# Kernel tuning notes

Measured on AMD Instinct MI355X. Metric: run time of the kernel, lower is better.

## Reference

```python
import jax, jax.numpy as jnp
import numpy as np

D_MODEL = 1024
NUM_HEADS = 16
D_K = D_MODEL // NUM_HEADS


def setup_inputs() -> dict:
    key = jax.random.key(0)
    ks = jax.random.split(key, 6)
    B, S = 2, 2048
    scale = 1.0 / np.sqrt(D_MODEL)
    x = jax.random.normal(ks[0], (B, S, D_MODEL), dtype=jnp.float32)
    w_q = jax.random.normal(ks[1], (D_MODEL, D_MODEL), dtype=jnp.float32) * scale
    w_k = jax.random.normal(ks[2], (D_MODEL, D_MODEL), dtype=jnp.float32) * scale
    w_v = jax.random.normal(ks[3], (D_MODEL, D_MODEL), dtype=jnp.float32) * scale
    w_o = jax.random.normal(ks[4], (D_MODEL, D_MODEL), dtype=jnp.float32) * scale
    b_o = jax.random.normal(ks[5], (D_MODEL,), dtype=jnp.float32) * 0.01
    return {"x": x, "w_q": w_q, "w_k": w_k, "w_v": w_v, "w_o": w_o, "b_o": b_o}


def reference(x, w_q, w_k, w_v, w_o, b_o):
    B, S, _ = x.shape
    # Linear(d, d, bias=False): y = x @ W.T ; weights stored torch-style [out, in]
    def proj(w):
        y = jnp.einsum('bsd,ed->bse', x, w)
        return y.reshape(B, S, NUM_HEADS, D_K).transpose(0, 2, 1, 3)  # [B,H,S,Dk]
    Q, K, V = proj(w_q), proj(w_k), proj(w_v)
    scores = jnp.einsum('bhqd,bhkd->bhqk', Q, K) / np.sqrt(D_K)
    attn = jax.nn.softmax(scores, axis=-1)  # dropout p=0 (eval) -> identity
    out = jnp.einsum('bhqk,bhkd->bhqd', attn, V)
    out = out.transpose(0, 2, 1, 3).reshape(B, S, D_MODEL)
    return jnp.einsum('bsd,ed->bse', out, w_o) + b_o
```

## Files before the change

### kernel.cpp

```cpp
#include <hip/hip_runtime.h>
#include <hip/hip_bf16.h>


typedef __bf16 bf16x8 __attribute__((ext_vector_type(8)));
typedef float f32x4 __attribute__((ext_vector_type(4)));
typedef float f32x16 __attribute__((ext_vector_type(16)));

__device__ __forceinline__ unsigned short f2bf(float f) {
  union { float f; unsigned int u; } c; c.f = f;
  unsigned int u = c.u;
  return (unsigned short)((u + 0x7FFFu + ((u >> 16) & 1u)) >> 16);
}

__device__ __forceinline__ unsigned int pk2bf(float a, float b) {
  union { float f; unsigned int u; } x, y;
  x.f = a; y.f = b;
  return __builtin_amdgcn_perm(y.u + 0x8000u, x.u + 0x8000u, 0x07060302u);
}

__device__ __forceinline__ bf16x8 ld_frag(const unsigned short* p) {
  union { uint4 u; bf16x8 b; } c;
  c.u = *(const uint4*)p;
  return c.b;
}

__device__ __forceinline__ uint4 cvt8(const float* __restrict__ p) {
  float4 a = *(const float4*)p;
  float4 b = *(const float4*)(p + 4);
  union { uint4 u; unsigned short s[8]; } r;
  r.s[0] = f2bf(a.x); r.s[1] = f2bf(a.y); r.s[2] = f2bf(a.z); r.s[3] = f2bf(a.w);
  r.s[4] = f2bf(b.x); r.s[5] = f2bf(b.y); r.s[6] = f2bf(b.z); r.s[7] = f2bf(b.w);
  return r.u;
}

typedef __attribute__((address_space(1))) const unsigned int as1_u32;
typedef __attribute__((address_space(3))) unsigned int as3_u32;
__device__ __forceinline__ void async16(const unsigned short* g,
                                        unsigned short* l) {
  __builtin_amdgcn_global_load_lds(
      (as1_u32*)(unsigned long long)g,
      (as3_u32*)(unsigned int)(unsigned long long)l, 16, 0, 0);
}

__global__ __launch_bounds__(256) void cvt_all(
    const float* __restrict__ s0, const float* __restrict__ s1,
    const float* __restrict__ s2, const float* __restrict__ s3,
    const float* __restrict__ s4,
    unsigned short* __restrict__ d0, unsigned short* __restrict__ d1,
    unsigned short* __restrict__ d2, unsigned short* __restrict__ d3,
    unsigned short* __restrict__ d4) {
  const float* srcs[5] = {s0, s1, s2, s3, s4};
  unsigned short* dsts[5] = {d0, d1, d2, d3, d4};
  const int ns[5] = {4194304, 1048576, 1048576, 1048576, 1048576};
  const int y = blockIdx.y;
  const int idx = (blockIdx.x * 256 + threadIdx.x) * 8;
  if (idx >= ns[y]) return;
  *(uint4*)(dsts[y] + idx) = cvt8(srcs[y] + idx);
}

template <int BM, bool OUT_F32>
__global__ __launch_bounds__(256, 3) void gemm_bt(
    const unsigned short* __restrict__ A,
    const unsigned short* __restrict__ w0,
    const unsigned short* __restrict__ w1,
    const unsigned short* __restrict__ w2,
    const float* __restrict__ bias,
    void* __restrict__ outraw, float z0scale) {
  constexpr int NT = (BM == 128) ? 4 : 2;
  constexpr int RA = BM / 4;
  const int z = blockIdx.z;
  const unsigned short* W = (z == 0) ? w0 : ((z == 1) ? w1 : w2);
  const float scl = (z == 0) ? z0scale : 1.0f;

  __shared__ unsigned short a_lds[BM * 64];
  __shared__ unsigned short b_lds[128 * 64];

  const int tid = threadIdx.x;
  const int wave = tid >> 6, lane = tid & 63;
  const int quad = lane >> 4, l16 = lane & 15;
  const int wm = (BM == 128) ? (wave >> 1) * 64 : 0;
  const int wn = (BM == 128) ? (wave & 1) * 64 : wave * 32;
  const int bm = blockIdx.x * BM, bn = blockIdx.y * 128;

  const int r8 = lane >> 3;
  const int sl = (lane & 7) ^ r8;
  const unsigned short* ga = A + (size_t)(bm + wave * RA + r8) * 1024 + sl * 8;
  const unsigned short* gb = W + (size_t)(bn + wave * 32 + r8) * 1024 + sl * 8;
  unsigned short* la = &a_lds[wave * RA * 64];
  unsigned short* lb = &b_lds[wave * 32 * 64];

  f32x4 acc[4][NT] = {};

  for (int k0 = 0; k0 < 1024; k0 += 64) {
#pragma unroll
    for (int c = 0; c < RA / 8; ++c)
      async16(ga + (size_t)c * 8 * 1024, la + c * 512);
#pragma unroll
    for (int c = 0; c < 4; ++c)
      async16(gb + (size_t)c * 8 * 1024, lb + c * 512);
    ga += 64; gb += 64;
    __syncthreads();

    bf16x8 af[2][4], bfr[2][NT];
#pragma unroll
    for (int kk = 0; kk < 2; ++kk) {
#pragma unroll
      for (int t = 0; t < 4; ++t) {
        const int row = wm + t * 16 + l16;
        af[kk][t] =
            ld_frag(&a_lds[row * 64 + (((kk * 4 + quad) ^ (row & 7)) * 8)]);
      }
#pragma unroll
      for (int t = 0; t < NT; ++t) {
        const int row = wn + t * 16 + l16;
        bfr[kk][t] =
            ld_frag(&b_lds[row * 64 + (((kk * 4 + quad) ^ (row & 7)) * 8)]);
      }
    }
#pragma unroll
    for (int kk = 0; kk < 2; ++kk)
#pragma unroll
      for (int mt = 0; mt < 4; ++mt)
#pragma unroll
        for (int nt = 0; nt < NT; ++nt)
          acc[mt][nt] = __builtin_amdgcn_mfma_f32_16x16x32_bf16(
              af[kk][mt], bfr[kk][nt], acc[mt][nt], 0, 0, 0);
    __syncthreads();
  }

#pragma unroll
  for (int nt = 0; nt < NT; ++nt) {
    const int n = bn + wn + nt * 16 + l16;
    const float bv = bias ? bias[n] : 0.0f;
#pragma unroll
    for (int mt = 0; mt < 4; ++mt)
#pragma unroll
      for (int r = 0; r < 4; ++r) {
        const int m = bm + wm + mt * 16 + quad * 4 + r;
        const float v = acc[mt][nt][r] * scl + bv;
        if (OUT_F32)
          ((float*)outraw)[(size_t)z * 4096 * 1024 + (size_t)m * 1024 + n] = v;
        else
          ((unsigned short*)outraw)[(size_t)z * 4096 * 1024 +
                                    (size_t)m * 1024 + n] = f2bf(v);
      }
  }
}

__global__ __launch_bounds__(256) void transpose_v(
    const unsigned short* __restrict__ v, unsigned short* __restrict__ vt) {
  const int st0 = blockIdx.x * 64;
  const int bh = blockIdx.y, b = bh >> 4, h = bh & 15;
  __shared__ unsigned short t[64 * 72];
  const int tid = threadIdx.x;
#pragma unroll
  for (int it = 0; it < 2; ++it) {
    const int c = it * 256 + tid;
    const int row = c >> 3, c8 = (c & 7) * 8;
    *(uint4*)&t[row * 72 + c8] =
        *(const uint4*)(v + (size_t)(b * 2048 + st0 + row) * 1024 + h * 64 + c8);
  }
  __syncthreads();
#pragma unroll
  for (int it = 0; it < 2; ++it) {
    const int c = it * 256 + tid;
    const int drow = c >> 3, s8 = (c & 7) * 8;
    union { uint4 u; unsigned short e[8]; } o;
#pragma unroll
    for (int j = 0; j < 8; ++j) o.e[j] = t[(s8 + j) * 72 + drow];
    *(uint4*)(vt + ((size_t)bh * 64 + drow) * 2048 + st0 + s8) = o.u;
  }
}

__global__ __launch_bounds__(256, 4) void attn4(
    const unsigned short* __restrict__ qkv,
    const unsigned short* __restrict__ vt_g,
    unsigned short* __restrict__ ab) {
  constexpr size_t PL = (size_t)4096 * 1024;
  const int qt = blockIdx.x, bh = blockIdx.y;
  const int b = bh >> 4, h = bh & 15;

  __shared__ __align__(16) unsigned short kvs[2][2][64 * 64];
  __shared__ float sm_l[2][2][32];

  const int tid = threadIdx.x;
  const int wave = tid >> 6, lane = tid & 63;
  const int ws = wave >> 1, wq = wave & 1;
  const int hi = lane >> 5, l32 = lane & 31;
  const int row8 = lane >> 3;
  const int sl = (lane & 7) ^ (row8 & 7);
  const int swz = (l32 & 7) * 8;

  const unsigned short* qrow =
      qkv + (size_t)(b * 2048 + qt * 64 + wq * 32 + l32) * 1024 + h * 64 +
      hi * 8;
  bf16x8 qf[4];
#pragma unroll
  for (int kc = 0; kc < 4; ++kc) qf[kc] = ld_frag(qrow + kc * 16);

  const unsigned short* gK =
      qkv + PL + (size_t)(b * 2048 + ws * 1024 + wq * 32 + row8) * 1024 +
      h * 64 + sl * 8;
  const unsigned short* gV =
      vt_g + (size_t)bh * 64 * 2048 + (size_t)(wq * 32 + row8) * 2048 +
      ws * 1024 + sl * 8;
  unsigned short* lK = &kvs[ws][0][wq * 4 * 512];
  unsigned short* lV = &kvs[ws][1][wq * 4 * 512];

  f32x16 o_acc[2] = {};
  float l_part = 0.0f;

  for (int t = 0; t < 16; ++t) {
#pragma unroll
    for (int c = 0; c < 4; ++c) {
      async16(gK + (size_t)c * 8 * 1024, lK + c * 512);
      async16(gV + (size_t)c * 8 * 2048, lV + c * 512);
    }
    gK += 64 * 1024;
    gV += 64;
    __syncthreads();

    f32x16 st[2] = {};
#pragma unroll
    for (int mb = 0; mb < 2; ++mb)
#pragma unroll
      for (int kc = 0; kc < 4; ++kc) {
        bf16x8 ak = ld_frag(
            &kvs[ws][0][(mb * 32 + l32) * 64 + (((2 * kc + hi) * 8) ^ swz)]);
        st[mb] = __builtin_amdgcn_mfma_f32_32x32x16_bf16(ak, qf[kc], st[mb],
                                                         0, 0, 0);
      }

    unsigned int u[2][4][2];
#pragma unroll
    for (int mb = 0; mb < 2; ++mb) {
#pragma unroll
      for (int r = 0; r < 16; ++r) {
        const float p = __builtin_amdgcn_exp2f(st[mb][r]);
        st[mb][r] = p;
        l_part += p;
      }
#pragma unroll
      for (int g = 0; g < 4; ++g) {
        u[mb][g][0] = pk2bf(st[mb][g * 4 + 0], st[mb][g * 4 + 1]);
        u[mb][g][1] = pk2bf(st[mb][g * 4 + 2], st[mb][g * 4 + 3]);
      }
    }

#pragma unroll
    for (int ks = 0; ks < 4; ++ks) {
      const int m = ks >> 1, g = (ks & 1) * 2;
      unsigned int a0 = u[m][g][0], b0 = u[m][g + 1][0];
      unsigned int a1 = u[m][g][1], b1 = u[m][g + 1][1];
      asm("v_permlane32_swap_b32 %0, %1" : "+v"(a0), "+v"(b0));
      asm("v_permlane32_swap_b32 %0, %1" : "+v"(a1), "+v"(b1));
      union { unsigned int w[4]; bf16x8 f; } pa;
      pa.w[0] = a0; pa.w[1] = a1; pa.w[2] = b0; pa.w[3] = b1;
#pragma unroll
      for (int nb = 0; nb < 2; ++nb) {
        bf16x8 bv = ld_frag(
            &kvs[ws][1][(nb * 32 + l32) * 64 + (((2 * ks + hi) * 8) ^ swz)]);
        o_acc[nb] = __builtin_amdgcn_mfma_f32_32x32x16_bf16(pa.f, bv,
                                                            o_acc[nb], 0, 0, 0);
      }
    }
    __syncthreads();
  }

  float lsum = l_part + __shfl_xor(l_part, 32);

  float* sm_o = (float*)&kvs[0][0][0];
  if (ws == 1) {
#pragma unroll
    for (int nb = 0; nb < 2; ++nb)
#pragma unroll
      for (int r = 0; r < 16; ++r) {
        const int q = (r & 3) + 8 * (r >> 2) + 4 * hi;
        sm_o[wq * 2048 + q * 64 + nb * 32 + l32] = o_acc[nb][r];
      }
  }
  if (lane < 32) sm_l[ws][wq][l32] = lsum;
  __syncthreads();

  if (ws == 0) {
#pragma unroll
    for (int r = 0; r < 16; ++r) {
      const int q = (r & 3) + 8 * (r >> 2) + 4 * hi;
      const float inv = 1.0f / (sm_l[0][wq][q] + sm_l[1][wq][q]);
      const size_t row = (size_t)(b * 2048 + qt * 64 + wq * 32 + q);
#pragma unroll
      for (int nb = 0; nb < 2; ++nb) {
        const float v =
            (o_acc[nb][r] + sm_o[wq * 2048 + q * 64 + nb * 32 + l32]) * inv;
        ab[row * 1024 + h * 64 + nb * 32 + l32] = f2bf(v);
      }
    }
  }
}

extern "C" void kernel_launch(void* const* d_in, const int* in_sizes, int n_in,
                              void* d_out, int out_size, void* d_ws,
                              size_t ws_size, hipStream_t stream) {
  const float* x  = (const float*)d_in[0];
  const float* wq = (const float*)d_in[1];
  const float* wk = (const float*)d_in[2];
  const float* wv = (const float*)d_in[3];
  const float* wo = (const float*)d_in[4];
  const float* bo = (const float*)d_in[5];

  constexpr size_t PL = (size_t)4096 * 1024;
  unsigned short* qkv = (unsigned short*)d_ws;
  unsigned short* ab  = qkv + 2 * PL;
  unsigned short* xb  = qkv + 3 * PL;
  unsigned short* vt  = xb;
  unsigned short* wqb = qkv + 4 * PL;
  unsigned short* wkb = wqb + 1024 * 1024;
  unsigned short* wvb = wkb + 1024 * 1024;
  unsigned short* wob = wvb + 1024 * 1024;

  const float QSCALE = 0.18033688011112042f;

  cvt_all<<<dim3(2048, 5), 256, 0, stream>>>(x, wq, wk, wv, wo,
                                             xb, wqb, wkb, wvb, wob);
  gemm_bt<128, false><<<dim3(32, 8, 3), 256, 0, stream>>>(
      xb, wqb, wkb, wvb, nullptr, qkv, QSCALE);
  transpose_v<<<dim3(32, 32), 256, 0, stream>>>(qkv + 2 * PL, vt);
  attn4<<<dim3(32, 32), 256, 0, stream>>>(qkv, vt, ab);
  gemm_bt<64, true><<<dim3(64, 8, 1), 256, 0, stream>>>(
      ab, wob, wob, wob, bo, d_out, 1.0f);
}
```

Baseline: 181.3 us.

## Fuse V transpose into QKV GEMM epilogue and register-prefetch attention K/V tiles

The QKV projection GEMM now writes the V slice directly in transposed [B,H,Dk,S] layout through an LDS staging tile in its epilogue, which removes the separate transpose_v kernel and its extra global round trip. The attention kernel replaces per-iteration async LDS copies with register prefetch of the next K/V tile, issued after the QK MFMAs and stored to LDS after a barrier. It also adds s_setprio hints around the MFMA blocks. This should overlap global loads with compute at the cost of more registers and a second barrier per iteration. The workspace layout is reshuffled so the attention output reuses the xb buffer.

```diff
diff --git a/kernel.cpp b/kernel.cpp
--- a/kernel.cpp
+++ b/kernel.cpp
@@ -72,8 +72,9 @@
   const unsigned short* W = (z == 0) ? w0 : ((z == 1) ? w1 : w2);
   const float scl = (z == 0) ? z0scale : 1.0f;
 
-  __shared__ unsigned short a_lds[BM * 64];
-  __shared__ unsigned short b_lds[128 * 64];
+  __shared__ unsigned short smem[(BM + 128) * 64];
+  unsigned short* a_lds = smem;
+  unsigned short* b_lds = smem + BM * 64;
 
   const int tid = threadIdx.x;
   const int wave = tid >> 6, lane = tid & 63;
@@ -124,8 +125,39 @@
 #pragma unroll
         for (int nt = 0; nt < NT; ++nt)
           acc[mt][nt] = __builtin_amdgcn_mfma_f32_16x16x32_bf16(
-              af[kk][mt], bfr[kk][nt], acc[mt][nt], 0, 0, 0);
+              af[kk][mt], bfr[kk][nt], acc[kk ? mt : mt][nt], 0, 0, 0),
+          acc[mt][nt] = acc[mt][nt];
     __syncthreads();
+  }
+
+  if (!OUT_F32 && BM == 128 && z == 2) {
+    unsigned short* tt = smem;
+#pragma unroll
+    for (int nt = 0; nt < NT; ++nt) {
+      const int nl = wn + nt * 16 + l16;
+#pragma unroll
+      for (int mt = 0; mt < 4; ++mt) {
+        const int ml = wm + mt * 16 + quad * 4;
+        union { uint2 u; unsigned short s[4]; } pk;
+#pragma unroll
+        for (int r = 0; r < 4; ++r) pk.s[r] = f2bf(acc[mt][nt][r]);
+        const int g = (ml >> 3) ^ (nl & 7);
+        *(uint2*)&tt[nl * 128 + g * 8 + (ml & 7)] = pk.u;
+      }
+    }
+    __syncthreads();
+    const int nl = tid >> 1, sc = (tid & 1) * 64;
+    const int bb = bm >> 11, s0 = bm & 2047;
+    const int hh = (bn >> 6) + (nl >> 6);
+    unsigned short* vtp = (unsigned short*)outraw + (size_t)2 * 4096 * 1024 +
+                          ((size_t)(bb * 16 + hh)) * 131072 +
+                          (size_t)(nl & 63) * 2048 + s0 + sc;
+#pragma unroll
+    for (int k = 0; k < 8; ++k) {
+      const int g = ((sc + k * 8) >> 3) ^ (nl & 7);
+      *(uint4*)&vtp[k * 8] = *(const uint4*)&tt[nl * 128 + g * 8];
+    }
+    return;
   }
 
 #pragma unroll
@@ -147,32 +179,7 @@
   }
 }
 
-__global__ __launch_bounds__(256) void transpose_v(
-    const unsigned short* __restrict__ v, unsigned short* __restrict__ vt) {
-  const int st0 = blockIdx.x * 64;
-  const int bh = blockIdx.y, b = bh >> 4, h = bh & 15;
-  __shared__ unsigned short t[64 * 72];
-  const int tid = threadIdx.x;
-#pragma unroll
-  for (int it = 0; it < 2; ++it) {
-    const int c = it * 256 + tid;
-    const int row = c >> 3, c8 = (c & 7) * 8;
-    *(uint4*)&t[row * 72 + c8] =
-        *(const uint4*)(v + (size_t)(b * 2048 + st0 + row) * 1024 + h * 64 + c8);
-  }
-  __syncthreads();
-#pragma unroll
-  for (int it = 0; it < 2; ++it) {
-    const int c = it * 256 + tid;
-    const int drow = c >> 3, s8 = (c & 7) * 8;
-    union { uint4 u; unsigned short e[8]; } o;
-#pragma unroll
-    for (int j = 0; j < 8; ++j) o.e[j] = t[(s8 + j) * 72 + drow];
-    *(uint4*)(vt + ((size_t)bh * 64 + drow) * 2048 + st0 + s8) = o.u;
-  }
-}
-
-__global__ __launch_bounds__(256, 4) void attn4(
+__global__ __launch_bounds__(256, 4) void attn6(
     const unsigned short* __restrict__ qkv,
     const unsigned short* __restrict__ vt_g,
     unsigned short* __restrict__ ab) {
@@ -210,17 +217,23 @@
   f32x16 o_acc[2] = {};
   float l_part = 0.0f;
 
+  uint4 pk_[4], pv_[4];
+#pragma unroll
+  for (int c = 0; c < 4; ++c) {
+    pk_[c] = *(const uint4*)(gK + (size_t)c * 8 * 1024);
+    pv_[c] = *(const uint4*)(gV + (size_t)c * 8 * 2048);
+  }
+  gK += 64 * 1024; gV += 64;
+#pragma unroll
+  for (int c = 0; c < 4; ++c) {
+    *(uint4*)(lK + c * 512 + lane * 8) = pk_[c];
+    *(uint4*)(lV + c * 512 + lane * 8) = pv_[c];
+  }
+  __syncthreads();
+
   for (int t = 0; t < 16; ++t) {
-#pragma unroll
-    for (int c = 0; c < 4; ++c) {
-      async16(gK + (size_t)c * 8 * 1024, lK + c * 512);
-      async16(gV + (size_t)c * 8 * 2048, lV + c * 512);
-    }
-    gK += 64 * 1024;
-    gV += 64;
-    __syncthreads();
-
     f32x16 st[2] = {};
+    __builtin_amdgcn_s_setprio(1);
 #pragma unroll
     for (int mb = 0; mb < 2; ++mb)
 #pragma unroll
@@ -230,6 +243,17 @@
         st[mb] = __builtin_amdgcn_mfma_f32_32x32x16_bf16(ak, qf[kc], st[mb],
                                                          0, 0, 0);
       }
+    __builtin_amdgcn_s_setprio(0);
+
+    if (t < 15) {
+#pragma unroll
+      for (int c = 0; c < 4; ++c) {
+        pk_[c] = *(const uint4*)(gK + (size_t)c * 8 * 1024);
+        pv_[c] = *(const uint4*)(gV + (size_t)c * 8 * 2048);
+      }
+      gK += 64 * 1024; gV += 64;
+      __builtin_amdgcn_sched_barrier(0);
+    }
 
     unsigned int u[2][4][2];
 #pragma unroll
@@ -256,6 +280,7 @@
       asm("v_permlane32_swap_b32 %0, %1" : "+v"(a1), "+v"(b1));
       union { unsigned int w[4]; bf16x8 f; } pa;
       pa.w[0] = a0; pa.w[1] = a1; pa.w[2] = b0; pa.w[3] = b1;
+      __builtin_amdgcn_s_setprio(1);
 #pragma unroll
       for (int nb = 0; nb < 2; ++nb) {
         bf16x8 bv = ld_frag(
@@ -263,8 +288,21 @@
         o_acc[nb] = __builtin_amdgcn_mfma_f32_32x32x16_bf16(pa.f, bv,
                                                             o_acc[nb], 0, 0, 0);
       }
-    }
-    __syncthreads();
+      __builtin_amdgcn_s_setprio(0);
+    }
+
+    asm volatile("s_waitcnt lgkmcnt(0)" ::: "memory");
+    __builtin_amdgcn_sched_barrier(0);
+    __builtin_amdgcn_s_barrier();
+
+    if (t < 15) {
+#pragma unroll
+      for (int c = 0; c < 4; ++c) {
+        *(uint4*)(lK + c * 512 + lane * 8) = pk_[c];
+        *(uint4*)(lV + c * 512 + lane * 8) = pv_[c];
+      }
+      __syncthreads();
+    }
   }
 
   float lsum = l_part + __shfl_xor(l_part, 32);
@@ -310,9 +348,8 @@
 
   constexpr size_t PL = (size_t)4096 * 1024;
   unsigned short* qkv = (unsigned short*)d_ws;
-  unsigned short* ab  = qkv + 2 * PL;
   unsigned short* xb  = qkv + 3 * PL;
-  unsigned short* vt  = xb;
+  unsigned short* ab  = xb;
   unsigned short* wqb = qkv + 4 * PL;
   unsigned short* wkb = wqb + 1024 * 1024;
   unsigned short* wvb = wkb + 1024 * 1024;
@@ -324,8 +361,7 @@
                                              xb, wqb, wkb, wvb, wob);
   gemm_bt<128, false><<<dim3(32, 8, 3), 256, 0, stream>>>(
       xb, wqb, wkb, wvb, nullptr, qkv, QSCALE);
-  transpose_v<<<dim3(32, 32), 256, 0, stream>>>(qkv + 2 * PL, vt);
-  attn4<<<dim3(32, 32), 256, 0, stream>>>(qkv, vt, ab);
+  attn6<<<dim3(32, 32), 256, 0, stream>>>(qkv, qkv + 2 * PL, ab);
   gemm_bt<64, true><<<dim3(64, 8, 1), 256, 0, stream>>>(
       ab, wob, wob, wob, bo, d_out, 1.0f);
 }
```

After: 293.0 us. 61.7% more time.
